# Optimization experiments

Measured on AMD Instinct MI355X. Metric: run time of the kernel, lower is better.

## Reference

```python
import jax, jax.numpy as jnp
import numpy as np

B, C, H, W = 8, 192, 128, 128
NUM_HEADS = 4
EPS = 1e-12  # torch F.normalize default eps
DN = ('NCHW', 'OIHW', 'NCHW')


def setup_inputs() -> dict:
    key = jax.random.key(0)
    k1, k2, k3, k4 = jax.random.split(key, 4)
    x = jax.random.normal(k1, (B, C, H, W), dtype=jnp.float32)
    qkv_w = jax.random.normal(k2, (3 * C, C, 1, 1), dtype=jnp.float32) * 0.05
    dw_w = jax.random.normal(k3, (3 * C, 1, 3, 3), dtype=jnp.float32) * 0.1
    proj_w = jax.random.normal(k4, (C, C, 1, 1), dtype=jnp.float32) * 0.05
    temperature = jnp.ones((NUM_HEADS, 1, 1), dtype=jnp.float32)
    return {"x": x, "qkv_w": qkv_w, "dw_w": dw_w, "proj_w": proj_w,
            "temperature": temperature}


def _l2norm(t):
    # F.normalize(t, dim=-1): divide by max(||t||, eps)
    n = jnp.sqrt(jnp.sum(t * t, axis=-1, keepdims=True))
    return t / jnp.maximum(n, EPS)


def reference(x, qkv_w, dw_w, proj_w, temperature):
    b, c, h, w = x.shape
    nh = NUM_HEADS
    cph = c // nh
    # 1x1 conv -> depthwise 3x3 conv (groups = 3*dim)
    qkv = jax.lax.conv_general_dilated(x, qkv_w, (1, 1), 'VALID',
                                       dimension_numbers=DN)
    qkv = jax.lax.conv_general_dilated(qkv, dw_w, (1, 1), [(1, 1), (1, 1)],
                                       dimension_numbers=DN,
                                       feature_group_count=3 * c)
    q, k, v = jnp.split(qkv, 3, axis=1)
    # [b, nh, cph, h*w]
    q = q.reshape(b, nh, cph, h * w)
    k = k.reshape(b, nh, cph, h * w)
    v = v.reshape(b, nh, cph, h * w)
    q = _l2norm(q)
    k = _l2norm(k)
    # channel attention: [b, nh, cph, cph]
    attn = jnp.einsum('bhcn,bhdn->bhcd', q, k) * temperature
    attn = jax.nn.softmax(attn, axis=-1)
    out = jnp.einsum('bhcd,bhdn->bhcn', attn, v)
    out = out.reshape(b, c, h, w)
    return jax.lax.conv_general_dilated(out, proj_w, (1, 1), 'VALID',
                                        dimension_numbers=DN)
```

## Files before the change

kernel.cpp:

```cpp
#include <hip/hip_runtime.h>
#include <hip/hip_bf16.h>

typedef __hip_bfloat16 bf16;
typedef __attribute__((ext_vector_type(8))) __bf16 bf16x8;
typedef __attribute__((ext_vector_type(4))) float f32x4;

#define HW 16384

static __device__ __forceinline__ float b2f(bf16 v) { return __bfloat162float(v); }
static __device__ __forceinline__ bf16 f2b(float v) { return __float2bfloat16(v); }
static __device__ __forceinline__ float blo(unsigned int w) {
    return __uint_as_float(w << 16);
}
static __device__ __forceinline__ float bhi(unsigned int w) {
    return __uint_as_float(w & 0xffff0000u);
}
static __device__ __forceinline__ unsigned short f2bu(float v) {
    union { bf16 b; unsigned short u; } c; c.b = f2b(v); return c.u;
}

static __device__ __forceinline__ void stf(float* p, float v) { *p = v; }
static __device__ __forceinline__ void stf(bf16* p, float v)  { *p = f2b(v); }

static __device__ __forceinline__ void load8(const float* p, float* v) {
    const float4* q = (const float4*)p;
    float4 a = q[0], b = q[1];
    v[0] = a.x; v[1] = a.y; v[2] = a.z; v[3] = a.w;
    v[4] = b.x; v[5] = b.y; v[6] = b.z; v[7] = b.w;
}
static __device__ __forceinline__ void load8(const bf16* p, float* v) {
    uint4 u = *(const uint4*)p;
    v[0] = blo(u.x); v[1] = bhi(u.x); v[2] = blo(u.y); v[3] = bhi(u.y);
    v[4] = blo(u.z); v[5] = bhi(u.z); v[6] = blo(u.w); v[7] = bhi(u.w);
}

template <typename TX, typename TY>
__global__ __launch_bounds__(256) void gemm_mfma(
    const float* __restrict__ Wm, const TX* __restrict__ X,
    TY* __restrict__ Y, int M, int K, int N)
{
    const int mb = blockIdx.x, nb = blockIdx.y, b = blockIdx.z;
    const TX* Xb = X + (size_t)b * K * N;
    TY* Yb = Y + (size_t)b * M * N;
    const int m0 = mb * 64, n0 = nb * 64;

    __shared__ __bf16 As[64][40];
    __shared__ __bf16 Bs[64][40];

    const int tid = threadIdx.x;
    const int lane = tid & 63, wave = tid >> 6;
    const int wm = (wave & 1) * 32, wn = (wave >> 1) * 32;
    const int r16 = lane & 15, quad = lane >> 4;

    f32x4 acc[2][2];
#pragma unroll
    for (int i = 0; i < 2; i++)
#pragma unroll
        for (int j = 0; j < 2; j++) acc[i][j] = (f32x4){0.f, 0.f, 0.f, 0.f};

    for (int k0 = 0; k0 < K; k0 += 32) {
        {
            int m = tid >> 2, kq = (tid & 3) * 8;
            float v[8];
            load8(Wm + (size_t)(m0 + m) * K + k0 + kq, v);
            bf16x8 pk;
#pragma unroll
            for (int j = 0; j < 8; j++) pk[j] = (__bf16)v[j];
            *(bf16x8*)&As[m][kq] = pk;
        }
        {
            int k = tid >> 3, n8 = (tid & 7) * 8;
            float v[8];
            load8(Xb + (size_t)(k0 + k) * N + n0 + n8, v);
#pragma unroll
            for (int j = 0; j < 8; j++) Bs[n8 + j][k] = (__bf16)v[j];
        }
        __syncthreads();
        bf16x8 a0 = *(const bf16x8*)&As[wm + r16][quad * 8];
        bf16x8 a1 = *(const bf16x8*)&As[wm + 16 + r16][quad * 8];
        bf16x8 b0 = *(const bf16x8*)&Bs[wn + r16][quad * 8];
        bf16x8 b1 = *(const bf16x8*)&Bs[wn + 16 + r16][quad * 8];
        acc[0][0] = __builtin_amdgcn_mfma_f32_16x16x32_bf16(a0, b0, acc[0][0], 0, 0, 0);
        acc[0][1] = __builtin_amdgcn_mfma_f32_16x16x32_bf16(a0, b1, acc[0][1], 0, 0, 0);
        acc[1][0] = __builtin_amdgcn_mfma_f32_16x16x32_bf16(a1, b0, acc[1][0], 0, 0, 0);
        acc[1][1] = __builtin_amdgcn_mfma_f32_16x16x32_bf16(a1, b1, acc[1][1], 0, 0, 0);
        __syncthreads();
    }

#pragma unroll
    for (int sm = 0; sm < 2; sm++)
#pragma unroll
        for (int sn = 0; sn < 2; sn++) {
            int gr = m0 + wm + sm * 16 + quad * 4;
            int gc = n0 + wn + sn * 16 + r16;
#pragma unroll
            for (int r = 0; r < 4; r++)
                stf(Yb + (size_t)(gr + r) * N + gc, acc[sm][sn][r]);
        }
}

__global__ __launch_bounds__(256) void dwconv3x3(
    const bf16* __restrict__ in, const float* __restrict__ wdw,
    bf16* __restrict__ out)
{
    const int plane = blockIdx.x >> 2;
    const int ybase = (blockIdx.x & 3) << 5;
    const int c = plane % 576;
    const bf16* ip = in + ((size_t)plane << 14);

    __shared__ unsigned short Ls[34][128];

    for (int i = threadIdx.x; i < 34 * 16; i += 256) {
        int r = i >> 4, cx = i & 15;
        int y = ybase - 1 + r;
        uint4 v = make_uint4(0u, 0u, 0u, 0u);
        if (y >= 0 && y < 128) v = ((const uint4*)(ip + ((size_t)y << 7)))[cx];
        ((uint4*)Ls[r])[cx] = v;
    }

    float w[9];
#pragma unroll
    for (int i = 0; i < 9; i++) w[i] = wdw[c * 9 + i];

    __syncthreads();

    const int lr = threadIdx.x >> 3;
    const int c0 = (threadIdx.x & 7) << 4;

    float row[3][18];
#pragma unroll
    for (int r3 = 0; r3 < 3; r3++) {
        int rr = lr + r3;
        row[r3][0]  = c0 ? blo((unsigned int)Ls[rr][c0 - 1] << 0) * 0.f + __uint_as_float((unsigned int)Ls[rr][c0 - 1] << 16) : 0.f;
        row[r3][17] = (c0 + 16 < 128) ? __uint_as_float((unsigned int)Ls[rr][c0 + 16] << 16) : 0.f;
        const uint4* rp = (const uint4*)&Ls[rr][c0];
        uint4 p0 = rp[0], p1 = rp[1];
        row[r3][1] = blo(p0.x); row[r3][2] = bhi(p0.x);
        row[r3][3] = blo(p0.y); row[r3][4] = bhi(p0.y);
        row[r3][5] = blo(p0.z); row[r3][6] = bhi(p0.z);
        row[r3][7] = blo(p0.w); row[r3][8] = bhi(p0.w);
        row[r3][9]  = blo(p1.x); row[r3][10] = bhi(p1.x);
        row[r3][11] = blo(p1.y); row[r3][12] = bhi(p1.y);
        row[r3][13] = blo(p1.z); row[r3][14] = bhi(p1.z);
        row[r3][15] = blo(p1.w); row[r3][16] = bhi(p1.w);
    }

    union { unsigned short s[16]; uint4 v[2]; } o;
#pragma unroll
    for (int j = 0; j < 16; j++) {
        float s = 0.f;
#pragma unroll
        for (int r3 = 0; r3 < 3; r3++)
            s += w[r3 * 3 + 0] * row[r3][j] + w[r3 * 3 + 1] * row[r3][j + 1]
               + w[r3 * 3 + 2] * row[r3][j + 2];
        o.s[j] = f2bu(s);
    }
    uint4* op = (uint4*)(out + ((size_t)plane << 14) + ((size_t)(ybase + lr) << 7) + c0);
    op[0] = o.v[0];
    op[1] = o.v[1];
}

__global__ __launch_bounds__(256) void rownorm(
    const bf16* __restrict__ qkv, float* __restrict__ rn)
{
    int r = blockIdx.x;
    int which = (r >= 1536) ? 1 : 0;
    int rr = r - which * 1536;
    int b = rr / 192, c = rr % 192;
    const bf16* p = qkv + ((size_t)(b * 576 + which * 192 + c) << 14);

    float s = 0.f;
    for (int i = threadIdx.x * 8; i < HW; i += 256 * 8) {
        float v[8];
        load8(p + i, v);
#pragma unroll
        for (int j = 0; j < 8; j++) s += v[j] * v[j];
    }
#pragma unroll
    for (int off = 32; off; off >>= 1) s += __shfl_down(s, off);
    __shared__ float red[4];
    if ((threadIdx.x & 63) == 0) red[threadIdx.x >> 6] = s;
    __syncthreads();
    if (threadIdx.x == 0) {
        float t = red[0] + red[1] + red[2] + red[3];
        rn[r] = 1.0f / fmaxf(sqrtf(t), 1e-12f);
    }
}

__global__ __launch_bounds__(256) void attn_dots(
    const bf16* __restrict__ qkv, float* __restrict__ attn)
{
    const int bh = blockIdx.y, b = bh >> 2, h = bh & 3;
    const int n0 = blockIdx.x * 1024;
    const bf16* q  = qkv + ((size_t)(b * 576 + h * 48) << 14);
    const bf16* kp = qkv + ((size_t)(b * 576 + 192 + h * 48) << 14);

    __shared__ float qt[48][68];
    __shared__ float kt[48][68];

    const int tid = threadIdx.x;
    const int cg = tid >> 4, dg = tid & 15;

    float acc[3][3] = {{0.f, 0.f, 0.f}, {0.f, 0.f, 0.f}, {0.f, 0.f, 0.f}};

    for (int s0 = 0; s0 < 1024; s0 += 64) {
        for (int i = tid; i < 48 * 8; i += 256) {
            int rowi = i / 8, cx = (i & 7) * 8;
            size_t off = ((size_t)rowi << 14) + n0 + s0 + cx;
            float v[8];
            load8(q + off, v);
#pragma unroll
            for (int j = 0; j < 8; j++) qt[rowi][cx + j] = v[j];
            load8(kp + off, v);
#pragma unroll
            for (int j = 0; j < 8; j++) kt[rowi][cx + j] = v[j];
        }
        __syncthreads();
#pragma unroll 8
        for (int n = 0; n < 64; n++) {
            float a0 = qt[cg * 3 + 0][n], a1 = qt[cg * 3 + 1][n], a2 = qt[cg * 3 + 2][n];
            float b0 = kt[dg * 3 + 0][n], b1 = kt[dg * 3 + 1][n], b2 = kt[dg * 3 + 2][n];
            acc[0][0] += a0 * b0; acc[0][1] += a0 * b1; acc[0][2] += a0 * b2;
            acc[1][0] += a1 * b0; acc[1][1] += a1 * b1; acc[1][2] += a1 * b2;
            acc[2][0] += a2 * b0; acc[2][1] += a2 * b1; acc[2][2] += a2 * b2;
        }
        __syncthreads();
    }
#pragma unroll
    for (int i = 0; i < 3; i++)
#pragma unroll
        for (int j = 0; j < 3; j++)
            atomicAdd(&attn[(size_t)bh * 2304 + (cg * 3 + i) * 48 + dg * 3 + j],
                      acc[i][j]);
}

__global__ __launch_bounds__(64) void softmax48(
    float* __restrict__ attn, const float* __restrict__ rn,
    const float* __restrict__ temp)
{
    int bh = blockIdx.x, b = bh >> 2, h = bh & 3;
    int c = threadIdx.x;
    if (c >= 48) return;
    float t = temp[h];
    float iq = rn[b * 192 + h * 48 + c];
    const float* ik = rn + 1536 + b * 192 + h * 48;
    float* row = attn + (size_t)bh * 2304 + c * 48;

    float v[48];
    float mx = -1e30f;
#pragma unroll
    for (int d = 0; d < 48; d++) {
        v[d] = row[d] * iq * ik[d] * t;
        mx = fmaxf(mx, v[d]);
    }
    float s = 0.f;
#pragma unroll
    for (int d = 0; d < 48; d++) {
        v[d] = expf(v[d] - mx);
        s += v[d];
    }
    float inv = 1.0f / s;
#pragma unroll
    for (int d = 0; d < 48; d++) row[d] = v[d] * inv;
}

__global__ __launch_bounds__(256) void attn_v(
    const float* __restrict__ attn, const bf16* __restrict__ qkv,
    bf16* __restrict__ outb)
{
    int bh = blockIdx.y, b = bh >> 2, h = bh & 3;
    int n = blockIdx.x * 256 + threadIdx.x;

    __shared__ float A[48 * 48];
    for (int i = threadIdx.x; i < 2304; i += 256) A[i] = attn[(size_t)bh * 2304 + i];
    __syncthreads();

    const bf16* v = qkv + ((size_t)(b * 576 + 384 + h * 48) << 14) + n;
    float acc[48];
#pragma unroll
    for (int c = 0; c < 48; c++) acc[c] = 0.f;

    for (int d = 0; d < 48; d++) {
        float vd = b2f(v[(size_t)d << 14]);
#pragma unroll
        for (int c = 0; c < 48; c++) acc[c] += A[c * 48 + d] * vd;
    }
    bf16* o = outb + ((size_t)(b * 192 + h * 48) << 14) + n;
#pragma unroll
    for (int c = 0; c < 48; c++) o[(size_t)c << 14] = f2b(acc[c]);
}

extern "C" void kernel_launch(void* const* d_in, const int* in_sizes, int n_in,
                              void* d_out, int out_size, void* d_ws, size_t ws_size,
                              hipStream_t stream)
{
    const float* x      = (const float*)d_in[0];
    const float* qkv_w  = (const float*)d_in[1];
    const float* dw_w   = (const float*)d_in[2];
    const float* proj_w = (const float*)d_in[3];
    const float* temp   = (const float*)d_in[4];
    float* out = (float*)d_out;

    char* ws = (char*)d_ws;
    const size_t qkvBytes = (size_t)8 * 576 * HW * sizeof(bf16);
    bf16*  qkv0 = (bf16*)ws;
    bf16*  qkv1 = (bf16*)(ws + qkvBytes);
    float* attn = (float*)(ws + 2 * qkvBytes);
    float* rn   = (float*)(ws + 2 * qkvBytes + (size_t)32 * 2304 * sizeof(float));
    bf16*  aout = qkv0;

    gemm_mfma<float, bf16><<<dim3(9, 256, 8), 256, 0, stream>>>(
        qkv_w, x, qkv0, 576, 192, HW);
    dwconv3x3<<<dim3(8 * 576 * 4), 256, 0, stream>>>(qkv0, dw_w, qkv1);
    rownorm<<<dim3(3072), 256, 0, stream>>>(qkv1, rn);
    hipMemsetAsync(attn, 0, (size_t)32 * 2304 * sizeof(float), stream);
    attn_dots<<<dim3(16, 32), 256, 0, stream>>>(qkv1, attn);
    softmax48<<<dim3(32), 64, 0, stream>>>(attn, rn, temp);
    attn_v<<<dim3(64, 32), 256, 0, stream>>>(attn, qkv1, aout);
    gemm_mfma<bf16, float><<<dim3(3, 256, 8), 256, 0, stream>>>(
        proj_w, aout, out, 192, 192, HW);
}
```

Measured before the change: 560.4 us.

## Use N-major bf16 operands for 1x1 convs and MFMA for attention dots

Adds a transpose-cast kernel that writes x as [b][n][k] in bf16. Replaces the K-looped GEMM with a single-stage kernel that loads the full K=192 tile of both operands into LDS and computes a 64x128 output tile, which removes the scattered transposed LDS stores and the per-K-step barriers. attn_v now writes its output in N-major layout so the projection GEMM reads it directly, and attn_dots switches from scalar FP32 FMAs to bf16 MFMA with per-wave LDS tiles. The cost is an extra transpose pass over x, much larger LDS use per block (lower occupancy), and bf16 rounding of q and k in the dot products.

```diff
diff --git a/kernel.cpp b/kernel.cpp
--- a/kernel.cpp
+++ b/kernel.cpp
@@ -18,7 +18,6 @@
 static __device__ __forceinline__ unsigned short f2bu(float v) {
     union { bf16 b; unsigned short u; } c; c.b = f2b(v); return c.u;
 }
-
 static __device__ __forceinline__ void stf(float* p, float v) { *p = v; }
 static __device__ __forceinline__ void stf(bf16* p, float v)  { *p = f2b(v); }
 
@@ -34,68 +33,97 @@
     v[4] = blo(u.z); v[5] = bhi(u.z); v[6] = blo(u.w); v[7] = bhi(u.w);
 }
 
-template <typename TX, typename TY>
-__global__ __launch_bounds__(256) void gemm_mfma(
-    const float* __restrict__ Wm, const TX* __restrict__ X,
-    TY* __restrict__ Y, int M, int K, int N)
+__global__ __launch_bounds__(256) void transpose_cast(
+    const float* __restrict__ x, bf16* __restrict__ xT)
+{
+    __shared__ float T[64][65];
+    const int k0 = blockIdx.x * 64, n0 = blockIdx.y * 64, b = blockIdx.z;
+    const float* xb = x + ((size_t)(b * 192 + k0) << 14) + n0;
+
+    for (int s = threadIdx.x; s < 64 * 16; s += 256) {
+        int k = s >> 4, n4 = (s & 15) * 4;
+        float4 v = *(const float4*)(xb + ((size_t)k << 14) + n4);
+        T[k][n4] = v.x; T[k][n4 + 1] = v.y; T[k][n4 + 2] = v.z; T[k][n4 + 3] = v.w;
+    }
+    __syncthreads();
+
+    bf16* xo = xT + ((size_t)b << 14) * 192 + (size_t)n0 * 192 + k0;
+    for (int s = threadIdx.x; s < 64 * 8; s += 256) {
+        int n = s >> 3, k8 = (s & 7) * 8;
+        union { unsigned short u[8]; uint4 v; } o;
+#pragma unroll
+        for (int j = 0; j < 8; j++) o.u[j] = f2bu(T[k8 + j][n]);
+        *(uint4*)(xo + (size_t)n * 192 + k8) = o.v;
+    }
+}
+
+template <typename TY>
+__global__ __launch_bounds__(256) void gemm_nk(
+    const float* __restrict__ Wm, const bf16* __restrict__ Bt,
+    TY* __restrict__ Y, int M, int N)
 {
     const int mb = blockIdx.x, nb = blockIdx.y, b = blockIdx.z;
-    const TX* Xb = X + (size_t)b * K * N;
+    const int m0 = mb * 64, n0 = nb * 128;
     TY* Yb = Y + (size_t)b * M * N;
-    const int m0 = mb * 64, n0 = nb * 64;
-
-    __shared__ __bf16 As[64][40];
-    __shared__ __bf16 Bs[64][40];
+    const bf16* Bb = Bt + ((size_t)b * N + n0) * 192;
+
+    __shared__ __bf16 As[64][200];
+    __shared__ __bf16 Bs[128][200];
 
     const int tid = threadIdx.x;
+    for (int s = tid; s < 64 * 24; s += 256) {
+        int m = s / 24, kq = (s % 24) * 8;
+        float v[8];
+        load8(Wm + (size_t)(m0 + m) * 192 + kq, v);
+        bf16x8 pk;
+#pragma unroll
+        for (int j = 0; j < 8; j++) pk[j] = (__bf16)v[j];
+        *(bf16x8*)&As[m][kq] = pk;
+    }
+    for (int s = tid; s < 128 * 24; s += 256) {
+        int n = s / 24, kq = s % 24;
+        *(uint4*)&Bs[n][kq * 8] = *(const uint4*)(Bb + (size_t)n * 192 + kq * 8);
+    }
+    __syncthreads();
+
     const int lane = tid & 63, wave = tid >> 6;
-    const int wm = (wave & 1) * 32, wn = (wave >> 1) * 32;
+    const int wm = (wave & 1) * 32, wn = (wave >> 1) * 64;
     const int r16 = lane & 15, quad = lane >> 4;
 
-    f32x4 acc[2][2];
+    f32x4 acc[2][4];
 #pragma unroll
     for (int i = 0; i < 2; i++)
 #pragma unroll
-        for (int j = 0; j < 2; j++) acc[i][j] = (f32x4){0.f, 0.f, 0.f, 0.f};
-
-    for (int k0 = 0; k0 < K; k0 += 32) {
-        {
-            int m = tid >> 2, kq = (tid & 3) * 8;
-            float v[8];
-            load8(Wm + (size_t)(m0 + m) * K + k0 + kq, v);
-            bf16x8 pk;
-#pragma unroll
-            for (int j = 0; j < 8; j++) pk[j] = (__bf16)v[j];
-            *(bf16x8*)&As[m][kq] = pk;
-        }
-        {
-            int k = tid >> 3, n8 = (tid & 7) * 8;
-            float v[8];
-            load8(Xb + (size_t)(k0 + k) * N + n0 + n8, v);
-#pragma unroll
-            for (int j = 0; j < 8; j++) Bs[n8 + j][k] = (__bf16)v[j];
-        }
-        __syncthreads();
-        bf16x8 a0 = *(const bf16x8*)&As[wm + r16][quad * 8];
-        bf16x8 a1 = *(const bf16x8*)&As[wm + 16 + r16][quad * 8];
-        bf16x8 b0 = *(const bf16x8*)&Bs[wn + r16][quad * 8];
-        bf16x8 b1 = *(const bf16x8*)&Bs[wn + 16 + r16][quad * 8];
+        for (int f = 0; f < 4; f++) acc[i][f] = (f32x4){0.f, 0.f, 0.f, 0.f};
+
+#pragma unroll
+    for (int kc = 0; kc < 6; kc++) {
+        const int kb = kc * 32 + quad * 8;
+        bf16x8 a0 = *(const bf16x8*)&As[wm + r16][kb];
+        bf16x8 a1 = *(const bf16x8*)&As[wm + 16 + r16][kb];
+        bf16x8 b0 = *(const bf16x8*)&Bs[wn + r16][kb];
+        bf16x8 b1 = *(const bf16x8*)&Bs[wn + 16 + r16][kb];
+        bf16x8 b2 = *(const bf16x8*)&Bs[wn + 32 + r16][kb];
+        bf16x8 b3 = *(const bf16x8*)&Bs[wn + 48 + r16][kb];
         acc[0][0] = __builtin_amdgcn_mfma_f32_16x16x32_bf16(a0, b0, acc[0][0], 0, 0, 0);
         acc[0][1] = __builtin_amdgcn_mfma_f32_16x16x32_bf16(a0, b1, acc[0][1], 0, 0, 0);
+        acc[0][2] = __builtin_amdgcn_mfma_f32_16x16x32_bf16(a0, b2, acc[0][2], 0, 0, 0);
+        acc[0][3] = __builtin_amdgcn_mfma_f32_16x16x32_bf16(a0, b3, acc[0][3], 0, 0, 0);
         acc[1][0] = __builtin_amdgcn_mfma_f32_16x16x32_bf16(a1, b0, acc[1][0], 0, 0, 0);
         acc[1][1] = __builtin_amdgcn_mfma_f32_16x16x32_bf16(a1, b1, acc[1][1], 0, 0, 0);
-        __syncthreads();
-    }
-
-#pragma unroll
-    for (int sm = 0; sm < 2; sm++)
-#pragma unroll
-        for (int sn = 0; sn < 2; sn++) {
-            int gr = m0 + wm + sm * 16 + quad * 4;
-            int gc = n0 + wn + sn * 16 + r16;
+        acc[1][2] = __builtin_amdgcn_mfma_f32_16x16x32_bf16(a1, b2, acc[1][2], 0, 0, 0);
+        acc[1][3] = __builtin_amdgcn_mfma_f32_16x16x32_bf16(a1, b3, acc[1][3], 0, 0, 0);
+    }
+
+#pragma unroll
+    for (int i = 0; i < 2; i++)
+#pragma unroll
+        for (int f = 0; f < 4; f++) {
+            int gr = m0 + wm + i * 16 + quad * 4;
+            int gc = n0 + wn + f * 16 + r16;
 #pragma unroll
             for (int r = 0; r < 4; r++)
-                stf(Yb + (size_t)(gr + r) * N + gc, acc[sm][sn][r]);
+                stf(Yb + (size_t)(gr + r) * N + gc, acc[i][f][r]);
         }
 }
 
@@ -131,7 +159,7 @@
 #pragma unroll
     for (int r3 = 0; r3 < 3; r3++) {
         int rr = lr + r3;
-        row[r3][0]  = c0 ? blo((unsigned int)Ls[rr][c0 - 1] << 0) * 0.f + __uint_as_float((unsigned int)Ls[rr][c0 - 1] << 16) : 0.f;
+        row[r3][0]  = c0 ? __uint_as_float((unsigned int)Ls[rr][c0 - 1] << 16) : 0.f;
         row[r3][17] = (c0 + 16 < 128) ? __uint_as_float((unsigned int)Ls[rr][c0 + 16] << 16) : 0.f;
         const uint4* rp = (const uint4*)&Ls[rr][c0];
         uint4 p0 = rp[0], p1 = rp[1];
@@ -191,47 +219,60 @@
     const bf16* __restrict__ qkv, float* __restrict__ attn)
 {
     const int bh = blockIdx.y, b = bh >> 2, h = bh & 3;
-    const int n0 = blockIdx.x * 1024;
+    const int tid = threadIdx.x;
+    const int wave = tid >> 6, lane = tid & 63;
+    const int n0 = blockIdx.x * 1024 + wave * 256;
     const bf16* q  = qkv + ((size_t)(b * 576 + h * 48) << 14);
     const bf16* kp = qkv + ((size_t)(b * 576 + 192 + h * 48) << 14);
 
-    __shared__ float qt[48][68];
-    __shared__ float kt[48][68];
-
-    const int tid = threadIdx.x;
-    const int cg = tid >> 4, dg = tid & 15;
-
-    float acc[3][3] = {{0.f, 0.f, 0.f}, {0.f, 0.f, 0.f}, {0.f, 0.f, 0.f}};
-
-    for (int s0 = 0; s0 < 1024; s0 += 64) {
-        for (int i = tid; i < 48 * 8; i += 256) {
-            int rowi = i / 8, cx = (i & 7) * 8;
-            size_t off = ((size_t)rowi << 14) + n0 + s0 + cx;
-            float v[8];
-            load8(q + off, v);
-#pragma unroll
-            for (int j = 0; j < 8; j++) qt[rowi][cx + j] = v[j];
-            load8(kp + off, v);
-#pragma unroll
-            for (int j = 0; j < 8; j++) kt[rowi][cx + j] = v[j];
+    __shared__ __bf16 S[4][2][48][72];
+
+    const int r16 = lane & 15, quad = lane >> 4;
+
+    f32x4 acc[3][3];
+#pragma unroll
+    for (int i = 0; i < 3; i++)
+#pragma unroll
+        for (int j = 0; j < 3; j++) acc[i][j] = (f32x4){0.f, 0.f, 0.f, 0.f};
+
+    for (int t = 0; t < 4; t++) {
+        const int nb = n0 + t * 64;
+        for (int s = lane; s < 48 * 8; s += 64) {
+            int c = s >> 3, seg = (s & 7) * 8;
+            *(uint4*)&S[wave][0][c][seg] = *(const uint4*)(q  + ((size_t)c << 14) + nb + seg);
+            *(uint4*)&S[wave][1][c][seg] = *(const uint4*)(kp + ((size_t)c << 14) + nb + seg);
         }
         __syncthreads();
-#pragma unroll 8
-        for (int n = 0; n < 64; n++) {
-            float a0 = qt[cg * 3 + 0][n], a1 = qt[cg * 3 + 1][n], a2 = qt[cg * 3 + 2][n];
-            float b0 = kt[dg * 3 + 0][n], b1 = kt[dg * 3 + 1][n], b2 = kt[dg * 3 + 2][n];
-            acc[0][0] += a0 * b0; acc[0][1] += a0 * b1; acc[0][2] += a0 * b2;
-            acc[1][0] += a1 * b0; acc[1][1] += a1 * b1; acc[1][2] += a1 * b2;
-            acc[2][0] += a2 * b0; acc[2][1] += a2 * b1; acc[2][2] += a2 * b2;
+#pragma unroll
+        for (int half = 0; half < 2; half++) {
+            const int kb = half * 32 + quad * 8;
+            bf16x8 qa[3], ka[3];
+#pragma unroll
+            for (int i = 0; i < 3; i++) {
+                qa[i] = *(const bf16x8*)&S[wave][0][i * 16 + r16][kb];
+                ka[i] = *(const bf16x8*)&S[wave][1][i * 16 + r16][kb];
+            }
+#pragma unroll
+            for (int i = 0; i < 3; i++)
+#pragma unroll
+                for (int j = 0; j < 3; j++)
+                    acc[i][j] = __builtin_amdgcn_mfma_f32_16x16x32_bf16(
+                        qa[i], ka[j], acc[i][j], 0, 0, 0);
         }
         __syncthreads();
     }
+
+    float* ap = attn + (size_t)bh * 2304;
 #pragma unroll
     for (int i = 0; i < 3; i++)
 #pragma unroll
-        for (int j = 0; j < 3; j++)
-            atomicAdd(&attn[(size_t)bh * 2304 + (cg * 3 + i) * 48 + dg * 3 + j],
-                      acc[i][j]);
+        for (int j = 0; j < 3; j++) {
+            int c = i * 16 + quad * 4;
+            int d = j * 16 + r16;
+#pragma unroll
+            for (int r = 0; r < 4; r++)
+                atomicAdd(&ap[(c + r) * 48 + d], acc[i][j][r]);
+        }
 }
 
 __global__ __launch_bounds__(64) void softmax48(
@@ -266,7 +307,7 @@
 
 __global__ __launch_bounds__(256) void attn_v(
     const float* __restrict__ attn, const bf16* __restrict__ qkv,
-    bf16* __restrict__ outb)
+    bf16* __restrict__ aout)
 {
     int bh = blockIdx.y, b = bh >> 2, h = bh & 3;
     int n = blockIdx.x * 256 + threadIdx.x;
@@ -285,9 +326,12 @@
 #pragma unroll
         for (int c = 0; c < 48; c++) acc[c] += A[c * 48 + d] * vd;
     }
-    bf16* o = outb + ((size_t)(b * 192 + h * 48) << 14) + n;
-#pragma unroll
-    for (int c = 0; c < 48; c++) o[(size_t)c << 14] = f2b(acc[c]);
+    union { unsigned short s[48]; uint4 v4[6]; } o;
+#pragma unroll
+    for (int c = 0; c < 48; c++) o.s[c] = f2bu(acc[c]);
+    uint4* op = (uint4*)(aout + (((size_t)b << 14) + n) * 192 + h * 48);
+#pragma unroll
+    for (int j = 0; j < 6; j++) op[j] = o.v4[j];
 }
 
 extern "C" void kernel_launch(void* const* d_in, const int* in_sizes, int n_in,
@@ -302,21 +346,21 @@
     float* out = (float*)d_out;
 
     char* ws = (char*)d_ws;
-    const size_t qkvBytes = (size_t)8 * 576 * HW * sizeof(bf16);
+    const size_t Q = (size_t)8 * 576 * HW * sizeof(bf16);
     bf16*  qkv0 = (bf16*)ws;
-    bf16*  qkv1 = (bf16*)(ws + qkvBytes);
-    float* attn = (float*)(ws + 2 * qkvBytes);
-    float* rn   = (float*)(ws + 2 * qkvBytes + (size_t)32 * 2304 * sizeof(float));
+    bf16*  qkv1 = (bf16*)(ws + Q);
+    bf16*  xT   = qkv1;
+    float* attn = (float*)(ws + 2 * Q);
+    float* rn   = (float*)(ws + 2 * Q + (size_t)32 * 2304 * sizeof(float));
     bf16*  aout = qkv0;
 
-    gemm_mfma<float, bf16><<<dim3(9, 256, 8), 256, 0, stream>>>(
-        qkv_w, x, qkv0, 576, 192, HW);
+    transpose_cast<<<dim3(3, 256, 8), 256, 0, stream>>>(x, xT);
+    gemm_nk<bf16><<<dim3(9, 128, 8), 256, 0, stream>>>(qkv_w, xT, qkv0, 576, HW);
     dwconv3x3<<<dim3(8 * 576 * 4), 256, 0, stream>>>(qkv0, dw_w, qkv1);
     rownorm<<<dim3(3072), 256, 0, stream>>>(qkv1, rn);
     hipMemsetAsync(attn, 0, (size_t)32 * 2304 * sizeof(float), stream);
     attn_dots<<<dim3(16, 32), 256, 0, stream>>>(qkv1, attn);
     softmax48<<<dim3(32), 64, 0, stream>>>(attn, rn, temp);
     attn_v<<<dim3(64, 32), 256, 0, stream>>>(attn, qkv1, aout);
-    gemm_mfma<bf16, float><<<dim3(3, 256, 8), 256, 0, stream>>>(
-        proj_w, aout, out, 192, 192, HW);
-}
+    gemm_nk<float><<<dim3(3, 128, 8), 256, 0, stream>>>(proj_w, aout, out, 192, HW);
+}
```

New measurement: 562.1 us. No clear change (+0.3%).
